# Kernel tuning notes

Measured on AMD Instinct MI355X. Metric: run time of the kernel, lower is better.

The kernel has to match this reference:

```python
import jax, jax.numpy as jnp
import numpy as np

ROWS, COLS, K = 32768, 2048, 512  # rows = 2*16*1024, K = normalized_size
EPS = 1e-5  # nn.LayerNorm default


def setup_inputs() -> dict:
    key = jax.random.key(0)
    k1, k2 = jax.random.split(key)
    x = jax.random.normal(k1, (2, 16, 1024, COLS), dtype=jnp.float32)
    gamma = jnp.ones((K,), dtype=jnp.float32)
    beta = jnp.zeros((K,), dtype=jnp.float32)
    # per-row random permutation prefix (distinct columns), vectorized via argsort of uniforms
    u = jax.random.uniform(k2, (ROWS, COLS))
    col_indices = jnp.argsort(u, axis=1)[:, :K].astype(jnp.int32)
    return {"x": x, "gamma": gamma, "beta": beta, "col_indices": col_indices}


def reference(x, gamma, beta, col_indices):
    shape = x.shape
    xf = x.reshape(-1, shape[-1])                       # [rows, cols]
    xg = jnp.take_along_axis(xf, col_indices, axis=1)   # [rows, K] random column gather
    # LayerNorm over last dim (biased variance, as torch)
    mu = jnp.mean(xg, axis=-1, keepdims=True)
    var = jnp.mean((xg - mu) ** 2, axis=-1, keepdims=True)
    xn = (xg - mu) * jax.lax.rsqrt(var + EPS) * gamma + beta
    xp = jax.nn.softmax(xn, axis=-1)
    # scatter back into zeros
    rows = jnp.arange(xf.shape[0])[:, None]
    out = jnp.zeros_like(xf).at[rows, col_indices].set(xp)
    return out.reshape(shape)
```

## Files before the change

### kernel.cpp

```cpp
#include <hip/hip_runtime.h>
#include <math.h>

constexpr int ROWS = 32768;
constexpr int COLS = 2048;
constexpr int K    = 512;
constexpr float EPS = 1e-5f;
constexpr int WPB  = 4;

typedef float f32x4 __attribute__((ext_vector_type(4)));
typedef int   i32x4 __attribute__((ext_vector_type(4)));

__device__ __forceinline__ void wave_lds_fence() {
    asm volatile("s_waitcnt lgkmcnt(0)" ::: "memory");
    __builtin_amdgcn_sched_barrier(0);
}

__global__ __launch_bounds__(256) void fused_gather_ln_softmax_scatter(
    const float* __restrict__ x,
    const float* __restrict__ gamma,
    const float* __restrict__ beta,
    const int*   __restrict__ cidx,
    float*       __restrict__ out)
{
    __shared__ float lds[WPB][COLS];
    const int lane = threadIdx.x & 63;
    const int wv   = threadIdx.x >> 6;
    const int row  = blockIdx.x * WPB + wv;

    f32x4* l4 = reinterpret_cast<f32x4*>(lds[wv]);
    const f32x4 z4 = (f32x4)(0.f);
    #pragma unroll
    for (int i = 0; i < 8; ++i)
        l4[i * 64 + lane] = z4;

    const i32x4* i4 = reinterpret_cast<const i32x4*>(cidx + (size_t)row * K) + lane * 2;
    const i32x4 ia = i4[0];
    const i32x4 ib = i4[1];
    const int idx[8] = {ia.x, ia.y, ia.z, ia.w, ib.x, ib.y, ib.z, ib.w};

    const f32x4* g4 = reinterpret_cast<const f32x4*>(gamma) + lane * 2;
    const f32x4* b4 = reinterpret_cast<const f32x4*>(beta)  + lane * 2;
    const f32x4 ga = g4[0], gb = g4[1];
    const f32x4 ba = b4[0], bb = b4[1];
    const float g[8] = {ga.x, ga.y, ga.z, ga.w, gb.x, gb.y, gb.z, gb.w};
    const float b[8] = {ba.x, ba.y, ba.z, ba.w, bb.x, bb.y, bb.z, bb.w};

    const float* xrow = x + (size_t)row * COLS;
    float v[8];
    #pragma unroll
    for (int j = 0; j < 8; ++j) v[j] = xrow[idx[j]];

    float s = 0.f, ss = 0.f;
    #pragma unroll
    for (int j = 0; j < 8; ++j) { s += v[j]; ss += v[j] * v[j]; }
    #pragma unroll
    for (int off = 32; off >= 1; off >>= 1) {
        s  += __shfl_xor(s,  off, 64);
        ss += __shfl_xor(ss, off, 64);
    }
    const float mu   = s * (1.f / K);
    const float var  = ss * (1.f / K) - mu * mu;
    const float rstd = rsqrtf(var + EPS);

    float xn[8];
    float m = -INFINITY;
    #pragma unroll
    for (int j = 0; j < 8; ++j) {
        xn[j] = (v[j] - mu) * rstd * g[j] + b[j];
        m = fmaxf(m, xn[j]);
    }
    #pragma unroll
    for (int off = 32; off >= 1; off >>= 1)
        m = fmaxf(m, __shfl_xor(m, off, 64));

    float p[8], ps = 0.f;
    #pragma unroll
    for (int j = 0; j < 8; ++j) { p[j] = __expf(xn[j] - m); ps += p[j]; }
    #pragma unroll
    for (int off = 32; off >= 1; off >>= 1)
        ps += __shfl_xor(ps, off, 64);
    const float inv = 1.f / ps;

    #pragma unroll
    for (int j = 0; j < 8; ++j)
        lds[wv][idx[j]] = p[j] * inv;

    wave_lds_fence();

    f32x4* o4 = reinterpret_cast<f32x4*>(out + (size_t)row * COLS);
    #pragma unroll
    for (int i = 0; i < 8; ++i)
        __builtin_nontemporal_store(l4[i * 64 + lane], &o4[i * 64 + lane]);
}

extern "C" void kernel_launch(void* const* d_in, const int* in_sizes, int n_in,
                              void* d_out, int out_size, void* d_ws, size_t ws_size,
                              hipStream_t stream) {
    const float* x     = (const float*)d_in[0];
    const float* gamma = (const float*)d_in[1];
    const float* beta  = (const float*)d_in[2];
    const int*   cidx  = (const int*)d_in[3];
    float* out = (float*)d_out;

    dim3 grid(ROWS / WPB);
    dim3 block(256);
    hipLaunchKernelGGL(fused_gather_ln_softmax_scatter, grid, block, 0, stream,
                       x, gamma, beta, cidx, out);
}
```

Before: 106.6 us.

## Stage full rows into LDS via async global_load_lds with double buffering

Each wave now handles four rows. It copies each whole x row into LDS with coalesced global_load_lds transfers and double-buffers them, so the next row's copy overlaps the current row's LayerNorm, softmax and scatter. The 512 random global gathers per row become LDS reads. Zeroing of the output buffer moves after the gather, and block size drops to two waves. This trades extra LDS traffic and hand-tuned vmcnt waits, which must also account for the outstanding stores, for fewer scattered global accesses and more memory-level parallelism.

After: 96.52 us. -9.4%, faster.

```diff
diff --git a/kernel.cpp b/kernel.cpp
--- a/kernel.cpp
+++ b/kernel.cpp
@@ -5,38 +5,52 @@
 constexpr int COLS = 2048;
 constexpr int K    = 512;
 constexpr float EPS = 1e-5f;
-constexpr int WPB  = 4;
+constexpr int WPB  = 2;
+constexpr int RPW  = 4;
 
 typedef float f32x4 __attribute__((ext_vector_type(4)));
 typedef int   i32x4 __attribute__((ext_vector_type(4)));
 
-__device__ __forceinline__ void wave_lds_fence() {
+__device__ __forceinline__ void sbar() { __builtin_amdgcn_sched_barrier(0); }
+
+__device__ __forceinline__ void lds_fence() {
     asm volatile("s_waitcnt lgkmcnt(0)" ::: "memory");
     __builtin_amdgcn_sched_barrier(0);
 }
 
-__global__ __launch_bounds__(256) void fused_gather_ln_softmax_scatter(
+#define VMWAIT(N) do { asm volatile("s_waitcnt vmcnt(" #N ")" ::: "memory"); \
+                       __builtin_amdgcn_sched_barrier(0); } while (0)
+
+__global__ __launch_bounds__(128) void fused_gather_ln_softmax_scatter(
     const float* __restrict__ x,
     const float* __restrict__ gamma,
     const float* __restrict__ beta,
     const int*   __restrict__ cidx,
     float*       __restrict__ out)
 {
-    __shared__ float lds[WPB][COLS];
+    __shared__ float lds[WPB * 2][COLS];
     const int lane = threadIdx.x & 63;
     const int wv   = threadIdx.x >> 6;
-    const int row  = blockIdx.x * WPB + wv;
+    const int gw   = blockIdx.x * WPB + wv;
+    const int row0 = gw * RPW;
 
-    f32x4* l4 = reinterpret_cast<f32x4*>(lds[wv]);
-    const f32x4 z4 = (f32x4)(0.f);
-    #pragma unroll
-    for (int i = 0; i < 8; ++i)
-        l4[i * 64 + lane] = z4;
+    float* bufA = lds[wv * 2 + 0];
+    float* bufB = lds[wv * 2 + 1];
 
-    const i32x4* i4 = reinterpret_cast<const i32x4*>(cidx + (size_t)row * K) + lane * 2;
-    const i32x4 ia = i4[0];
-    const i32x4 ib = i4[1];
-    const int idx[8] = {ia.x, ia.y, ia.z, ia.w, ib.x, ib.y, ib.z, ib.w};
+    auto dma_row = [&](float* buf, int row) {
+        const f32x4* src = reinterpret_cast<const f32x4*>(x + (size_t)row * COLS);
+        #pragma unroll
+        for (int ii = 0; ii < 8; ++ii)
+            __builtin_amdgcn_global_load_lds(
+                reinterpret_cast<const unsigned int*>(src + ii * 64 + lane),
+                reinterpret_cast<unsigned int*>(buf + ii * 256),
+                16, 0, 0);
+    };
+    auto idx_load = [&](i32x4& a, i32x4& b, int row) {
+        const i32x4* ip = reinterpret_cast<const i32x4*>(cidx + (size_t)row * K) + lane * 2;
+        a = __builtin_nontemporal_load(ip);
+        b = __builtin_nontemporal_load(ip + 1);
+    };
 
     const f32x4* g4 = reinterpret_cast<const f32x4*>(gamma) + lane * 2;
     const f32x4* b4 = reinterpret_cast<const f32x4*>(beta)  + lane * 2;
@@ -45,52 +59,77 @@
     const float g[8] = {ga.x, ga.y, ga.z, ga.w, gb.x, gb.y, gb.z, gb.w};
     const float b[8] = {ba.x, ba.y, ba.z, ba.w, bb.x, bb.y, bb.z, bb.w};
 
-    const float* xrow = x + (size_t)row * COLS;
-    float v[8];
-    #pragma unroll
-    for (int j = 0; j < 8; ++j) v[j] = xrow[idx[j]];
+    auto process = [&](float* buf, const i32x4 ia, const i32x4 ib, int row) {
+        const int idx[8] = {ia.x, ia.y, ia.z, ia.w, ib.x, ib.y, ib.z, ib.w};
+        float v[8];
+        #pragma unroll
+        for (int j = 0; j < 8; ++j) v[j] = buf[idx[j]];
 
-    float s = 0.f, ss = 0.f;
-    #pragma unroll
-    for (int j = 0; j < 8; ++j) { s += v[j]; ss += v[j] * v[j]; }
-    #pragma unroll
-    for (int off = 32; off >= 1; off >>= 1) {
-        s  += __shfl_xor(s,  off, 64);
-        ss += __shfl_xor(ss, off, 64);
-    }
-    const float mu   = s * (1.f / K);
-    const float var  = ss * (1.f / K) - mu * mu;
-    const float rstd = rsqrtf(var + EPS);
+        float s = 0.f, ss = 0.f;
+        #pragma unroll
+        for (int j = 0; j < 8; ++j) { s += v[j]; ss += v[j] * v[j]; }
+        #pragma unroll
+        for (int off = 32; off >= 1; off >>= 1) {
+            s  += __shfl_xor(s,  off, 64);
+            ss += __shfl_xor(ss, off, 64);
+        }
+        const float mu   = s * (1.f / K);
+        const float var  = ss * (1.f / K) - mu * mu;
+        const float rstd = rsqrtf(var + EPS);
 
-    float xn[8];
-    float m = -INFINITY;
-    #pragma unroll
-    for (int j = 0; j < 8; ++j) {
-        xn[j] = (v[j] - mu) * rstd * g[j] + b[j];
-        m = fmaxf(m, xn[j]);
-    }
-    #pragma unroll
-    for (int off = 32; off >= 1; off >>= 1)
-        m = fmaxf(m, __shfl_xor(m, off, 64));
+        float xn[8];
+        float m = -INFINITY;
+        #pragma unroll
+        for (int j = 0; j < 8; ++j) {
+            xn[j] = (v[j] - mu) * rstd * g[j] + b[j];
+            m = fmaxf(m, xn[j]);
+        }
+        #pragma unroll
+        for (int off = 32; off >= 1; off >>= 1)
+            m = fmaxf(m, __shfl_xor(m, off, 64));
 
-    float p[8], ps = 0.f;
-    #pragma unroll
-    for (int j = 0; j < 8; ++j) { p[j] = __expf(xn[j] - m); ps += p[j]; }
-    #pragma unroll
-    for (int off = 32; off >= 1; off >>= 1)
-        ps += __shfl_xor(ps, off, 64);
-    const float inv = 1.f / ps;
+        float p[8], ps = 0.f;
+        #pragma unroll
+        for (int j = 0; j < 8; ++j) { p[j] = __expf(xn[j] - m); ps += p[j]; }
+        #pragma unroll
+        for (int off = 32; off >= 1; off >>= 1)
+            ps += __shfl_xor(ps, off, 64);
+        const float inv = 1.f / ps;
 
-    #pragma unroll
-    for (int j = 0; j < 8; ++j)
-        lds[wv][idx[j]] = p[j] * inv;
+        f32x4* l4 = reinterpret_cast<f32x4*>(buf);
+        const f32x4 z4 = (f32x4)(0.f);
+        #pragma unroll
+        for (int i = 0; i < 8; ++i) l4[i * 64 + lane] = z4;
+        #pragma unroll
+        for (int j = 0; j < 8; ++j) buf[idx[j]] = p[j] * inv;
 
-    wave_lds_fence();
+        lds_fence();
 
-    f32x4* o4 = reinterpret_cast<f32x4*>(out + (size_t)row * COLS);
-    #pragma unroll
-    for (int i = 0; i < 8; ++i)
-        __builtin_nontemporal_store(l4[i * 64 + lane], &o4[i * 64 + lane]);
+        f32x4* o4 = reinterpret_cast<f32x4*>(out + (size_t)row * COLS);
+        #pragma unroll
+        for (int i = 0; i < 8; ++i)
+            __builtin_nontemporal_store(l4[i * 64 + lane], &o4[i * 64 + lane]);
+    };
+
+    i32x4 a0, b0, a1, b1, a2, b2, a3, b3;
+    idx_load(a0, b0, row0 + 0);
+    dma_row(bufA, row0 + 0);
+    sbar();
+
+    dma_row(bufB, row0 + 1); idx_load(a1, b1, row0 + 1); sbar();
+    VMWAIT(10);
+    process(bufA, a0, b0, row0 + 0); sbar();
+
+    dma_row(bufA, row0 + 2); idx_load(a2, b2, row0 + 2); sbar();
+    VMWAIT(18);
+    process(bufB, a1, b1, row0 + 1); sbar();
+
+    dma_row(bufB, row0 + 3); idx_load(a3, b3, row0 + 3); sbar();
+    VMWAIT(18);
+    process(bufA, a2, b2, row0 + 2); sbar();
+
+    VMWAIT(8);
+    process(bufB, a3, b3, row0 + 3); sbar();
 }
 
 extern "C" void kernel_launch(void* const* d_in, const int* in_sizes, int n_in,
@@ -102,8 +141,8 @@
     const int*   cidx  = (const int*)d_in[3];
     float* out = (float*)d_out;
 
-    dim3 grid(ROWS / WPB);
-    dim3 block(256);
+    dim3 grid(ROWS / (WPB * RPW));
+    dim3 block(WPB * 64);
     hipLaunchKernelGGL(fused_gather_ln_softmax_scatter, grid, block, 0, stream,
                        x, gamma, beta, cidx, out);
 }
```

## Stage full rows into LDS via async DMA and process several rows per wave

Applied to the files above, without the earlier changes.

Each wave now handles 8 consecutive rows instead of one. For each row it streams the whole x row into LDS with global_load_lds, so the random column gather happens in LDS rather than as scattered global loads. The DMA for the next row and its index loads are issued before the current row's output stores, overlapping them with the current row's work. The cost is reading every x column instead of just the gathered ones, a grid 8x smaller with fewer waves per CU, and hand-written vmcnt waits that must match the exact count of outstanding memory operations.

Measured after the change: 99.14 us. 7.0% less time.

```diff
diff --git a/kernel.cpp b/kernel.cpp
--- a/kernel.cpp
+++ b/kernel.cpp
@@ -6,14 +6,19 @@
 constexpr int K    = 512;
 constexpr float EPS = 1e-5f;
 constexpr int WPB  = 4;
+constexpr int RPW  = 8;
 
 typedef float f32x4 __attribute__((ext_vector_type(4)));
 typedef int   i32x4 __attribute__((ext_vector_type(4)));
+
+__device__ __forceinline__ void sbar() { __builtin_amdgcn_sched_barrier(0); }
 
 __device__ __forceinline__ void wave_lds_fence() {
     asm volatile("s_waitcnt lgkmcnt(0)" ::: "memory");
     __builtin_amdgcn_sched_barrier(0);
 }
+#define VMWAIT(N) do { asm volatile("s_waitcnt vmcnt(" #N ")" ::: "memory"); \
+                       __builtin_amdgcn_sched_barrier(0); } while (0)
 
 __global__ __launch_bounds__(256) void fused_gather_ln_softmax_scatter(
     const float* __restrict__ x,
@@ -25,18 +30,26 @@
     __shared__ float lds[WPB][COLS];
     const int lane = threadIdx.x & 63;
     const int wv   = threadIdx.x >> 6;
-    const int row  = blockIdx.x * WPB + wv;
+    const int gw   = blockIdx.x * WPB + wv;
+    const int row0 = gw * RPW;
 
-    f32x4* l4 = reinterpret_cast<f32x4*>(lds[wv]);
-    const f32x4 z4 = (f32x4)(0.f);
-    #pragma unroll
-    for (int i = 0; i < 8; ++i)
-        l4[i * 64 + lane] = z4;
+    float* buf = lds[wv];
+    f32x4* l4  = reinterpret_cast<f32x4*>(buf);
 
-    const i32x4* i4 = reinterpret_cast<const i32x4*>(cidx + (size_t)row * K) + lane * 2;
-    const i32x4 ia = i4[0];
-    const i32x4 ib = i4[1];
-    const int idx[8] = {ia.x, ia.y, ia.z, ia.w, ib.x, ib.y, ib.z, ib.w};
+    auto dma_row = [&](int r) {
+        const f32x4* src = reinterpret_cast<const f32x4*>(x + (size_t)(row0 + r) * COLS);
+        #pragma unroll
+        for (int ii = 0; ii < 8; ++ii)
+            __builtin_amdgcn_global_load_lds(
+                reinterpret_cast<const unsigned int*>(src + ii * 64 + lane),
+                reinterpret_cast<unsigned int*>(buf + ii * 256),
+                16, 0, 0);
+    };
+    auto idx_load = [&](int r, i32x4& a, i32x4& b) {
+        const i32x4* ip = reinterpret_cast<const i32x4*>(cidx + (size_t)(row0 + r) * K) + lane * 2;
+        a = __builtin_nontemporal_load(ip);
+        b = __builtin_nontemporal_load(ip + 1);
+    };
 
     const f32x4* g4 = reinterpret_cast<const f32x4*>(gamma) + lane * 2;
     const f32x4* b4 = reinterpret_cast<const f32x4*>(beta)  + lane * 2;
@@ -45,52 +58,81 @@
     const float g[8] = {ga.x, ga.y, ga.z, ga.w, gb.x, gb.y, gb.z, gb.w};
     const float b[8] = {ba.x, ba.y, ba.z, ba.w, bb.x, bb.y, bb.z, bb.w};
 
-    const float* xrow = x + (size_t)row * COLS;
-    float v[8];
-    #pragma unroll
-    for (int j = 0; j < 8; ++j) v[j] = xrow[idx[j]];
-
-    float s = 0.f, ss = 0.f;
-    #pragma unroll
-    for (int j = 0; j < 8; ++j) { s += v[j]; ss += v[j] * v[j]; }
-    #pragma unroll
-    for (int off = 32; off >= 1; off >>= 1) {
-        s  += __shfl_xor(s,  off, 64);
-        ss += __shfl_xor(ss, off, 64);
-    }
-    const float mu   = s * (1.f / K);
-    const float var  = ss * (1.f / K) - mu * mu;
-    const float rstd = rsqrtf(var + EPS);
-
-    float xn[8];
-    float m = -INFINITY;
-    #pragma unroll
-    for (int j = 0; j < 8; ++j) {
-        xn[j] = (v[j] - mu) * rstd * g[j] + b[j];
-        m = fmaxf(m, xn[j]);
-    }
-    #pragma unroll
-    for (int off = 32; off >= 1; off >>= 1)
-        m = fmaxf(m, __shfl_xor(m, off, 64));
-
-    float p[8], ps = 0.f;
-    #pragma unroll
-    for (int j = 0; j < 8; ++j) { p[j] = __expf(xn[j] - m); ps += p[j]; }
-    #pragma unroll
-    for (int off = 32; off >= 1; off >>= 1)
-        ps += __shfl_xor(ps, off, 64);
-    const float inv = 1.f / ps;
+    i32x4 ia, ib, na, nb;
+    dma_row(0);
+    idx_load(0, ia, ib);
+    sbar();
+    VMWAIT(0);
 
     #pragma unroll
-    for (int j = 0; j < 8; ++j)
-        lds[wv][idx[j]] = p[j] * inv;
+    for (int r = 0; r < RPW; ++r) {
+        const int idx[8] = {ia.x, ia.y, ia.z, ia.w, ib.x, ib.y, ib.z, ib.w};
 
-    wave_lds_fence();
+        float v[8];
+        #pragma unroll
+        for (int j = 0; j < 8; ++j) v[j] = buf[idx[j]];
 
-    f32x4* o4 = reinterpret_cast<f32x4*>(out + (size_t)row * COLS);
-    #pragma unroll
-    for (int i = 0; i < 8; ++i)
-        __builtin_nontemporal_store(l4[i * 64 + lane], &o4[i * 64 + lane]);
+        float s = 0.f, ss = 0.f;
+        #pragma unroll
+        for (int j = 0; j < 8; ++j) { s += v[j]; ss += v[j] * v[j]; }
+        #pragma unroll
+        for (int off = 32; off >= 1; off >>= 1) {
+            s  += __shfl_xor(s,  off, 64);
+            ss += __shfl_xor(ss, off, 64);
+        }
+        const float mu   = s * (1.f / K);
+        const float var  = ss * (1.f / K) - mu * mu;
+        const float rstd = rsqrtf(var + EPS);
+
+        float xn[8];
+        float m = -INFINITY;
+        #pragma unroll
+        for (int j = 0; j < 8; ++j) {
+            xn[j] = (v[j] - mu) * rstd * g[j] + b[j];
+            m = fmaxf(m, xn[j]);
+        }
+        #pragma unroll
+        for (int off = 32; off >= 1; off >>= 1)
+            m = fmaxf(m, __shfl_xor(m, off, 64));
+
+        float p[8], ps = 0.f;
+        #pragma unroll
+        for (int j = 0; j < 8; ++j) { p[j] = __expf(xn[j] - m); ps += p[j]; }
+        #pragma unroll
+        for (int off = 32; off >= 1; off >>= 1)
+            ps += __shfl_xor(ps, off, 64);
+        const float inv = 1.f / ps;
+
+        const f32x4 z4 = (f32x4)(0.f);
+        #pragma unroll
+        for (int i = 0; i < 8; ++i) l4[i * 64 + lane] = z4;
+        #pragma unroll
+        for (int j = 0; j < 8; ++j) buf[idx[j]] = p[j] * inv;
+
+        wave_lds_fence();
+
+        f32x4 o[8];
+        #pragma unroll
+        for (int i = 0; i < 8; ++i) o[i] = l4[i * 64 + lane];
+
+        wave_lds_fence();
+
+        if (r + 1 < RPW) {
+            dma_row(r + 1);
+            idx_load(r + 1, na, nb);
+        }
+        sbar();
+
+        f32x4* o4 = reinterpret_cast<f32x4*>(out + (size_t)(row0 + r) * COLS);
+        #pragma unroll
+        for (int i = 0; i < 8; ++i)
+            __builtin_nontemporal_store(o[i], &o4[i * 64 + lane]);
+
+        if (r + 1 < RPW) {
+            VMWAIT(8);
+            ia = na; ib = nb;
+        }
+    }
 }
 
 extern "C" void kernel_launch(void* const* d_in, const int* in_sizes, int n_in,
@@ -102,7 +144,7 @@
     const int*   cidx  = (const int*)d_in[3];
     float* out = (float*)d_out;
 
-    dim3 grid(ROWS / WPB);
+    dim3 grid(ROWS / (WPB * RPW));
     dim3 block(256);
     hipLaunchKernelGGL(fused_gather_ln_softmax_scatter, grid, block, 0, stream,
                        x, gamma, beta, cidx, out);
```
